# Kernel tuning notes

Hardware: AMD Instinct MI355X
Metric: run time of the kernel (lower is better)

Reference implementation:

```python
import jax, jax.numpy as jnp
import numpy as np

# ---- MERU-style Lorentz geometry helpers (space components, implicit time) ----

def _time(x, curv):
    # x: [..., D] space component; time = sqrt(1/curv + ||x||^2)
    return jnp.sqrt(1.0 / curv + jnp.sum(x * x, axis=-1))


def pairwise_dist(x, y, curv, eps=1e-8):
    # Lorentzian inner product for all pairs: <x,y>_L = x.y - x_t*y_t  -> [N, M]
    xt = _time(x, curv)
    yt = _time(y, curv)
    inner = jnp.einsum('nd,md->nm', x, y) - xt[:, None] * yt[None, :]
    c_xyl = -curv * inner  # >= 1 on the hyperboloid
    return jnp.arccosh(jnp.clip(c_xyl, 1.0 + eps, None)) / jnp.sqrt(curv)


def oxy_angle(x, y, curv, eps=1e-8):
    # exterior angle at x of geodesic triangle (origin, x, y); elementwise over batch
    xt = _time(x, curv)
    yt = _time(y, curv)
    c_xyl = curv * (jnp.sum(x * y, axis=-1) - xt * yt)  # <= -1
    acos_numer = yt + c_xyl * xt
    acos_denom = jnp.linalg.norm(x, axis=-1) * jnp.sqrt(jnp.clip(c_xyl * c_xyl - 1.0, 0.0, None))
    acos_input = acos_numer / (acos_denom + eps)
    return jnp.arccos(jnp.clip(acos_input, -1.0 + eps, 1.0 - eps))


def half_aperture(x, curv, min_radius=0.1, eps=1e-6):
    asin_input = 2.0 * min_radius / (jnp.linalg.norm(x, axis=-1) * jnp.sqrt(curv) + eps)
    return jnp.arcsin(jnp.clip(asin_input, -1.0 + eps, 1.0 - eps))


def soft_cross_entropy(logits, target_probs):
    # torch.nn.CrossEntropyLoss with probability targets (rows need not sum to 1)
    return jnp.mean(-jnp.sum(target_probs * jax.nn.log_softmax(logits, axis=-1), axis=-1))


def entailment_loss(fa, fb, curv, eps=1e-6):
    ang = oxy_angle(fa, fb, curv)
    ap = half_aperture(fa, curv, eps=eps)
    return jnp.mean(jnp.clip(ang - ap, 0.0, None))


def setup_inputs() -> dict:
    key = jax.random.key(0)
    k1, k2, k3, k4 = jax.random.split(key, 4)
    B, D = 4096, 512
    return {
        'image_features': jax.random.normal(k1, (B, D), dtype=jnp.float32),
        'dna_features': jax.random.normal(k2, (B, D), dtype=jnp.float32),
        'text_features': jax.random.normal(k3, (B, D), dtype=jnp.float32),
        'labels': jax.random.randint(k4, (B,), 0, 500, dtype=jnp.int64),
        'logit_scale': jnp.float32(10.0),
        'curv': jnp.float32(1.0),
    }


ENTAIL_WEIGHT = 0.2


def reference(image_features, dna_features, text_features, labels, logit_scale, curv):
    # world_size == 1: gathered features == local features
    label_mat = (labels[None, :] == labels[:, None]).astype(jnp.float32)  # [B, B]

    feats = [image_features, dna_features, text_features]  # idx 0=image, 1=dna, 2=text

    contrastive_losses = []
    entail_losses = []
    for ia in range(3):
        for ib in range(3):
            if ia == ib:
                continue
            sim_ab = -pairwise_dist(feats[ia], feats[ib], curv)
            sim_ba = -pairwise_dist(feats[ib], feats[ia], curv)
            contrastive_losses.append(soft_cross_entropy(logit_scale * sim_ab, label_mat))
            contrastive_losses.append(soft_cross_entropy(logit_scale * sim_ba, label_mat))
            # 2D features branch: entailment only for (dna, image) ordering
            if ia == 1 and ib == 0:
                entail_losses.append(entailment_loss(feats[1], feats[0], curv, eps=1e-6))
            elif ia == 0 and ib == 1:
                entail_losses.append(entailment_loss(feats[1], feats[0], curv, eps=1e-6))

    contrastive_total = sum(contrastive_losses) / len(contrastive_losses)
    entail_total = sum(entail_losses) / len(entail_losses)
    total = contrastive_total + ENTAIL_WEIGHT * entail_total
    return total, contrastive_total, entail_total
```

## Files before the change

### kernel.cpp

```cpp
#include <hip/hip_runtime.h>
#include <stdint.h>

#define B_SZ 4096
#define D_SZ 512
#define SHIFT 64.0f

typedef __attribute__((ext_vector_type(4))) float floatx4;
typedef __attribute__((ext_vector_type(2))) long lng2;
typedef unsigned char u8;
typedef unsigned int u32;

#define GLD_LDS16(gp, sp)                                                              \
    __builtin_amdgcn_global_load_lds(                                                  \
        (const __attribute__((address_space(1))) void*)(gp),                           \
        (__attribute__((address_space(3))) void*)(sp), 16, 0, 0)

#define FP8MFMA(accv, av, bv)                                                          \
    accv = __builtin_amdgcn_mfma_f32_16x16x32_fp8_fp8(av, bv, accv, 0, 0, 0)

__global__ __launch_bounds__(256) void prep_kernel(
    const float* __restrict__ img, const float* __restrict__ dna,
    const float* __restrict__ txt, const float* __restrict__ curv_p,
    const int* __restrict__ labels, int* __restrict__ hist,
    u8* __restrict__ f8, float* __restrict__ times,
    float* __restrict__ zero_f, float* __restrict__ ent_partial) {
    __shared__ int lhist[512];
    __shared__ float red[4];
    int t = threadIdx.x;
    int gid = blockIdx.x * 256 + t;
    if (gid < 49155) zero_f[gid] = 0.0f;

    if (blockIdx.x == 0) {
        lhist[t] = 0; lhist[t + 256] = 0;
        __syncthreads();
        for (int n = t; n < B_SZ; n += 256) atomicAdd(&lhist[labels[n]], 1);
        __syncthreads();
        hist[t] = lhist[t]; hist[t + 256] = lhist[t + 256];
    }

    int wave = gid >> 6;
    int lane = t & 63;
    const float* src = (wave < B_SZ) ? img : (wave < 2 * B_SZ) ? dna : txt;
    int row = wave & (B_SZ - 1);
    const float* p = src + row * D_SZ + lane * 8;
    float4 v0 = *(const float4*)(p);
    float4 v1 = *(const float4*)(p + 4);
    float ss = v0.x*v0.x + v0.y*v0.y + v0.z*v0.z + v0.w*v0.w
             + v1.x*v1.x + v1.y*v1.y + v1.z*v1.z + v1.w*v1.w;
    u32 w0 = __builtin_amdgcn_cvt_pk_fp8_f32(v0.x, v0.y, 0, false);
    w0 = __builtin_amdgcn_cvt_pk_fp8_f32(v0.z, v0.w, w0, true);
    u32 w1 = __builtin_amdgcn_cvt_pk_fp8_f32(v1.x, v1.y, 0, false);
    w1 = __builtin_amdgcn_cvt_pk_fp8_f32(v1.z, v1.w, w1, true);
    uint2 pk; pk.x = w0; pk.y = w1;
    int gperm = (lane & 56) | ((lane & 3) << 1) | ((lane >> 2) & 1);
    *(uint2*)(f8 + (size_t)wave * D_SZ + gperm * 8) = pk;

    bool isdna = (wave >= B_SZ) && (wave < 2 * B_SZ);
    float dot = 0.0f, ssy = 0.0f;
    if (isdna) {
        const float* y = img + row * D_SZ + lane * 8;
        float4 y0 = *(const float4*)y, y1 = *(const float4*)(y + 4);
        dot = v0.x*y0.x + v0.y*y0.y + v0.z*y0.z + v0.w*y0.w
            + v1.x*y1.x + v1.y*y1.y + v1.z*y1.z + v1.w*y1.w;
        ssy = y0.x*y0.x + y0.y*y0.y + y0.z*y0.z + y0.w*y0.w
            + y1.x*y1.x + y1.y*y1.y + y1.z*y1.z + y1.w*y1.w;
    }
    #pragma unroll
    for (int m = 1; m < 64; m <<= 1) {
        ss += __shfl_xor(ss, m);
        if (isdna) { dot += __shfl_xor(dot, m); ssy += __shfl_xor(ssy, m); }
    }
    float curv = curv_p[0];
    float ep = 0.0f;
    if (lane == 0) {
        float xt = sqrtf(1.0f / curv + ss);
        times[wave] = xt;
        if (isdna) {
            float yt = sqrtf(1.0f / curv + ssy);
            float nx = sqrtf(ss);
            float c = curv * (dot - xt * yt);
            float numer = yt + c * xt;
            float denom = nx * sqrtf(fmaxf(c * c - 1.0f, 0.0f));
            float ai = numer / (denom + 1e-8f);
            ai = fminf(fmaxf(ai, -1.0f + 1e-8f), 1.0f - 1e-8f);
            float ang = acosf(ai);
            float as_in = 0.2f / (nx * sqrtf(curv) + 1e-6f);
            as_in = fminf(fmaxf(as_in, -1.0f + 1e-6f), 1.0f - 1e-6f);
            float ap = asinf(as_in);
            ep = fmaxf(ang - ap, 0.0f);
        }
    }
    if (blockIdx.x >= 1024 && blockIdx.x < 2048) {
        if (lane == 0) red[t >> 6] = ep;
        __syncthreads();
        if (t == 0) ent_partial[blockIdx.x - 1024] = red[0] + red[1] + red[2] + red[3];
    }
}

__global__ __launch_bounds__(512, 4) void gemm_epi_kernel(
    const u8* __restrict__ f8, const float* __restrict__ times,
    const int* __restrict__ labels,
    const float* __restrict__ ls_p, const float* __restrict__ curv_p,
    float* __restrict__ rsum_e, float* __restrict__ rsum_t,
    float* __restrict__ csum_e, float* __restrict__ csum_t) {
    __shared__ u8 sA[2][128 * 64];
    __shared__ u8 sB[2][128 * 64];

    int z = blockIdx.z;
    int pa = (z == 2) ? 1 : 0;
    int pb = (z == 0) ? 1 : 2;
    const u8* A  = f8 + (size_t)pa * (B_SZ * D_SZ);
    const u8* Bm = f8 + (size_t)pb * (B_SZ * D_SZ);

    int t = threadIdx.x;
    int rowBlk = blockIdx.y * 128;
    int colBlk = blockIdx.x * 128;
    int wave = t >> 6, lane = t & 63;
    int wr = wave >> 1;
    int wc = wave & 1;

    int chunk = (t & 3) ^ ((t >> 3) & 3);
    const u8* gA = A  + (size_t)(rowBlk + (t >> 2)) * D_SZ + chunk * 16;
    const u8* gB = Bm + (size_t)(colBlk + (t >> 2)) * D_SZ + chunk * 16;

    int q = lane >> 4, s = lane & 15;
    int slot16 = (q ^ ((s >> 1) & 3)) << 4;
    int aBase = (wr * 32 + s) * 64 + slot16;
    int bBase = (wc * 64 + s) * 64 + slot16;

    floatx4 acc[2][4];
    #pragma unroll
    for (int ii = 0; ii < 2; ++ii)
        #pragma unroll
        for (int j = 0; j < 4; ++j) acc[ii][j] = (floatx4){0.f, 0.f, 0.f, 0.f};

    {
        GLD_LDS16(gA, &sA[0][wave * 1024]);
        GLD_LDS16(gB, &sB[0][wave * 1024]);
    }

    #pragma unroll
    for (int si = 0; si < D_SZ / 64; ++si) {
        const int cur = si & 1;
        __syncthreads();
        if (si < D_SZ / 64 - 1) {
            const int ko = (si + 1) * 64;
            GLD_LDS16(gA + ko, &sA[cur ^ 1][wave * 1024]);
            GLD_LDS16(gB + ko, &sB[cur ^ 1][wave * 1024]);
        }
        const u8* pA = &sA[cur][0];
        const u8* pB = &sB[cur][0];
        lng2 a0 = *(const lng2*)(pA + aBase);
        lng2 a1 = *(const lng2*)(pA + aBase + 1024);
        lng2 b0 = *(const lng2*)(pB + bBase);
        lng2 b1 = *(const lng2*)(pB + bBase + 1024);
        lng2 b2 = *(const lng2*)(pB + bBase + 2048);
        lng2 b3 = *(const lng2*)(pB + bBase + 3072);
        FP8MFMA(acc[0][0], a0.x, b0.x); FP8MFMA(acc[0][1], a0.x, b1.x);
        FP8MFMA(acc[0][2], a0.x, b2.x); FP8MFMA(acc[0][3], a0.x, b3.x);
        FP8MFMA(acc[1][0], a1.x, b0.x); FP8MFMA(acc[1][1], a1.x, b1.x);
        FP8MFMA(acc[1][2], a1.x, b2.x); FP8MFMA(acc[1][3], a1.x, b3.x);
        FP8MFMA(acc[0][0], a0.y, b0.y); FP8MFMA(acc[0][1], a0.y, b1.y);
        FP8MFMA(acc[0][2], a0.y, b2.y); FP8MFMA(acc[0][3], a0.y, b3.y);
        FP8MFMA(acc[1][0], a1.y, b0.y); FP8MFMA(acc[1][1], a1.y, b1.y);
        FP8MFMA(acc[1][2], a1.y, b2.y); FP8MFMA(acc[1][3], a1.y, b3.y);
    }

    float ls = ls_p[0];
    float curv = curv_p[0];
    float rsc = rsqrtf(curv);
    float c2 = -ls * rsc;
    float c1 = c2 * 0.69314718f;
    float sh2p = SHIFT * 1.44269504f + c2;
    const float* tA = times + pa * B_SZ;
    const float* tB = times + pb * B_SZ;

    int rowbase = rowBlk + wr * 32;
    int colbase = colBlk + wc * 64;

    float tb[4]; int lb[4]; int mcol[4];
    #pragma unroll
    for (int j = 0; j < 4; ++j) {
        mcol[j] = colbase + j * 16 + s;
        tb[j] = tB[mcol[j]];
        lb[j] = labels[mcol[j]];
    }
    float colE[4] = {0.f, 0.f, 0.f, 0.f}, colT[4] = {0.f, 0.f, 0.f, 0.f};

    float* rsE = rsum_e + z * B_SZ;
    float* rsT = rsum_t + z * B_SZ;
    float* csE = csum_e + z * B_SZ;
    float* csT = csum_t + z * B_SZ;

    #pragma unroll
    for (int ii = 0; ii < 2; ++ii) {
        int nb = rowbase + ii * 16 + q * 4;
        float cta[4]; int la[4];
        #pragma unroll
        for (int r = 0; r < 4; ++r) { cta[r] = curv * tA[nb + r]; la[r] = labels[nb + r]; }
        float re[4] = {0.f, 0.f, 0.f, 0.f}, rt[4] = {0.f, 0.f, 0.f, 0.f};
        #pragma unroll
        for (int j = 0; j < 4; ++j) {
            floatx4 a = acc[ii][j];
            #pragma unroll
            for (int r = 0; r < 4; ++r) {
                float zc = fmaf(-curv, a[r], cta[r] * tb[j]);
                zc = fmaxf(zc, 1.0f + 1e-8f);
                float lz = __log2f(zc);
                float e = __builtin_amdgcn_exp2f(fmaf(c2, lz, sh2p));
                float tl = (la[r] == lb[j]) ? fmaf(c1, lz, c1) : 0.0f;
                re[r] += e; rt[r] += tl;
                colE[j] += e; colT[j] += tl;
            }
        }
        #pragma unroll
        for (int r = 0; r < 4; ++r) {
            #pragma unroll
            for (int m = 1; m <= 8; m <<= 1) {
                re[r] += __shfl_xor(re[r], m);
                rt[r] += __shfl_xor(rt[r], m);
            }
        }
        #pragma unroll
        for (int r = 0; r < 4; ++r) {
            if (s == r) {
                atomicAdd(&rsE[nb + r], re[r]);
                atomicAdd(&rsT[nb + r], rt[r]);
            }
        }
    }
    #pragma unroll
    for (int j = 0; j < 4; ++j) {
        colE[j] += __shfl_xor(colE[j], 16); colE[j] += __shfl_xor(colE[j], 32);
        colT[j] += __shfl_xor(colT[j], 16); colT[j] += __shfl_xor(colT[j], 32);
        if (q == 0) {
            atomicAdd(&csE[mcol[j]], colE[j]);
            atomicAdd(&csT[mcol[j]], colT[j]);
        }
    }
}

__global__ __launch_bounds__(256) void finalize_kernel(
    const float* __restrict__ rsum_e, const float* __restrict__ rsum_t,
    const float* __restrict__ csum_e, const float* __restrict__ csum_t,
    const int* __restrict__ labels, const int* __restrict__ hist,
    const float* __restrict__ ent_partial,
    float* __restrict__ ce_acc, float* __restrict__ ent_acc,
    int* __restrict__ done, float* __restrict__ out) {
    __shared__ float red[4], red2[4];
    int b = blockIdx.x, tid = threadIdx.x;
    int n = b * 256 + tid;
    float Sn = (float)hist[labels[n]];
    float part = 0.0f;
    #pragma unroll
    for (int p = 0; p < 3; ++p) {
        part += Sn * (__logf(rsum_e[p * B_SZ + n]) - SHIFT) - rsum_t[p * B_SZ + n];
        part += Sn * (__logf(csum_e[p * B_SZ + n]) - SHIFT) - csum_t[p * B_SZ + n];
    }
    float ep = (b < 4) ? ent_partial[b * 256 + tid] : 0.0f;
    #pragma unroll
    for (int m = 1; m < 64; m <<= 1) {
        part += __shfl_xor(part, m);
        ep   += __shfl_xor(ep, m);
    }
    if ((tid & 63) == 0) { red[tid >> 6] = part; red2[tid >> 6] = ep; }
    __syncthreads();
    if (tid == 0) {
        atomicAdd(ce_acc, red[0] + red[1] + red[2] + red[3]);
        atomicAdd(ent_acc, red2[0] + red2[1] + red2[2] + red2[3]);
        __threadfence();
        if (atomicAdd(done, 1) == 15) {
            float ce = atomicAdd(ce_acc, 0.0f);
            float ent = atomicAdd(ent_acc, 0.0f);
            float contr = ce / (6.0f * (float)B_SZ);
            ent /= (float)B_SZ;
            out[0] = contr + 0.2f * ent;
            out[1] = contr;
            out[2] = ent;
        }
    }
}

extern "C" void kernel_launch(void* const* d_in, const int* in_sizes, int n_in,
                              void* d_out, int out_size, void* d_ws, size_t ws_size,
                              hipStream_t stream) {
    const float* img    = (const float*)d_in[0];
    const float* dna    = (const float*)d_in[1];
    const float* txt    = (const float*)d_in[2];
    const int*   labels = (const int*)d_in[3];
    const float* ls     = (const float*)d_in[4];
    const float* curv   = (const float*)d_in[5];

    char* ws = (char*)d_ws;
    u8*    f8     = (u8*)ws;
    float* times  = (float*)(ws + 6291456);
    float* rsum_e = (float*)(ws + 6340608);
    float* rsum_t = (float*)(ws + 6389760);
    float* csum_e = (float*)(ws + 6438912);
    float* csum_t = (float*)(ws + 6488064);
    float* ce_acc = (float*)(ws + 6537216);
    float* ent_acc= (float*)(ws + 6537220);
    int*   done   = (int*)  (ws + 6537224);
    float* ent_p  = (float*)(ws + 6537228);
    int*   hist   = (int*)  (ws + 6541324);

    prep_kernel<<<3072, 256, 0, stream>>>(img, dna, txt, curv, labels, hist,
                                          f8, times, rsum_e, ent_p);
    dim3 g(32, 32, 3);
    gemm_epi_kernel<<<g, 512, 0, stream>>>(f8, times, labels, ls, curv,
                                           rsum_e, rsum_t, csum_e, csum_t);
    finalize_kernel<<<16, 256, 0, stream>>>(rsum_e, rsum_t, csum_e, csum_t,
                                            labels, hist, ent_p,
                                            ce_acc, ent_acc, done, (float*)d_out);
}
```

Baseline: 168.1 us.

## Load GEMM operands directly from global memory instead of staging through LDS

Removes the double-buffered LDS staging (global_load_lds plus __syncthreads) and has each wave read its fp8 A/B fragments straight from global memory into registers. It also drops the occupancy hint from launch bounds. This is meant to remove barrier and LDS traffic overhead, but each tile is now re-read from global/L2 by multiple waves, which costs more memory traffic and leaves no software prefetch to hide latency.

```diff
diff --git a/kernel.cpp b/kernel.cpp
--- a/kernel.cpp
+++ b/kernel.cpp
@@ -9,11 +9,6 @@
 typedef __attribute__((ext_vector_type(2))) long lng2;
 typedef unsigned char u8;
 typedef unsigned int u32;
-
-#define GLD_LDS16(gp, sp)                                                              \
-    __builtin_amdgcn_global_load_lds(                                                  \
-        (const __attribute__((address_space(1))) void*)(gp),                           \
-        (__attribute__((address_space(3))) void*)(sp), 16, 0, 0)
 
 #define FP8MFMA(accv, av, bv)                                                          \
     accv = __builtin_amdgcn_mfma_f32_16x16x32_fp8_fp8(av, bv, accv, 0, 0, 0)
@@ -97,15 +92,12 @@
     }
 }
 
-__global__ __launch_bounds__(512, 4) void gemm_epi_kernel(
+__global__ __launch_bounds__(512) void gemm_epi_kernel(
     const u8* __restrict__ f8, const float* __restrict__ times,
     const int* __restrict__ labels,
     const float* __restrict__ ls_p, const float* __restrict__ curv_p,
     float* __restrict__ rsum_e, float* __restrict__ rsum_t,
     float* __restrict__ csum_e, float* __restrict__ csum_t) {
-    __shared__ u8 sA[2][128 * 64];
-    __shared__ u8 sB[2][128 * 64];
-
     int z = blockIdx.z;
     int pa = (z == 2) ? 1 : 0;
     int pb = (z == 0) ? 1 : 2;
@@ -119,14 +111,10 @@
     int wr = wave >> 1;
     int wc = wave & 1;
 
-    int chunk = (t & 3) ^ ((t >> 3) & 3);
-    const u8* gA = A  + (size_t)(rowBlk + (t >> 2)) * D_SZ + chunk * 16;
-    const u8* gB = Bm + (size_t)(colBlk + (t >> 2)) * D_SZ + chunk * 16;
-
     int q = lane >> 4, s = lane & 15;
-    int slot16 = (q ^ ((s >> 1) & 3)) << 4;
-    int aBase = (wr * 32 + s) * 64 + slot16;
-    int bBase = (wc * 64 + s) * 64 + slot16;
+
+    const u8* fA = A  + (size_t)(rowBlk + wr * 32 + s) * D_SZ + q * 16;
+    const u8* fB = Bm + (size_t)(colBlk + wc * 64 + s) * D_SZ + q * 16;
 
     floatx4 acc[2][4];
     #pragma unroll
@@ -134,28 +122,15 @@
         #pragma unroll
         for (int j = 0; j < 4; ++j) acc[ii][j] = (floatx4){0.f, 0.f, 0.f, 0.f};
 
-    {
-        GLD_LDS16(gA, &sA[0][wave * 1024]);
-        GLD_LDS16(gB, &sB[0][wave * 1024]);
-    }
-
     #pragma unroll
     for (int si = 0; si < D_SZ / 64; ++si) {
-        const int cur = si & 1;
-        __syncthreads();
-        if (si < D_SZ / 64 - 1) {
-            const int ko = (si + 1) * 64;
-            GLD_LDS16(gA + ko, &sA[cur ^ 1][wave * 1024]);
-            GLD_LDS16(gB + ko, &sB[cur ^ 1][wave * 1024]);
-        }
-        const u8* pA = &sA[cur][0];
-        const u8* pB = &sB[cur][0];
-        lng2 a0 = *(const lng2*)(pA + aBase);
-        lng2 a1 = *(const lng2*)(pA + aBase + 1024);
-        lng2 b0 = *(const lng2*)(pB + bBase);
-        lng2 b1 = *(const lng2*)(pB + bBase + 1024);
-        lng2 b2 = *(const lng2*)(pB + bBase + 2048);
-        lng2 b3 = *(const lng2*)(pB + bBase + 3072);
+        const int ko = si * 64;
+        lng2 a0 = *(const lng2*)(fA + ko);
+        lng2 a1 = *(const lng2*)(fA + 16 * D_SZ + ko);
+        lng2 b0 = *(const lng2*)(fB + ko);
+        lng2 b1 = *(const lng2*)(fB + 16 * D_SZ + ko);
+        lng2 b2 = *(const lng2*)(fB + 32 * D_SZ + ko);
+        lng2 b3 = *(const lng2*)(fB + 48 * D_SZ + ko);
         FP8MFMA(acc[0][0], a0.x, b0.x); FP8MFMA(acc[0][1], a0.x, b1.x);
         FP8MFMA(acc[0][2], a0.x, b2.x); FP8MFMA(acc[0][3], a0.x, b3.x);
         FP8MFMA(acc[1][0], a1.x, b0.x); FP8MFMA(acc[1][1], a1.x, b1.x);
```

New measurement: 242.0 us. +43.9%, slower.
